# Optimization experiments

Measured on AMD Instinct MI355X. Metric: run time of the kernel, lower is better.

Reference implementation:

```python
import jax, jax.numpy as jnp
import numpy as np

N, C, H, T, D, K = 4096, 512, 128, 64, 20, 10


def setup_inputs() -> dict:
    key = jax.random.key(0)
    ks = jax.random.split(key, 40)
    s = 0.05
    inp = {}
    inp["x"] = jax.random.normal(ks[0], (N, D * T), jnp.float32)
    inp["concept_matrix"] = (jax.random.uniform(ks[1], (N, C)) < 0.05).astype(jnp.float32)
    inp["market_value"] = jax.random.uniform(ks[2], (N,), jnp.float32) + 0.1
    # GRU params (torch layout: w_ih [3H,in], w_hh [3H,H], biases [3H]); 2 layers
    inp["gru_w_ih0"] = jax.random.normal(ks[3], (3 * H, D), jnp.float32) * s
    inp["gru_w_hh0"] = jax.random.normal(ks[4], (3 * H, H), jnp.float32) * s
    inp["gru_b_ih0"] = jax.random.normal(ks[5], (3 * H,), jnp.float32) * s
    inp["gru_b_hh0"] = jax.random.normal(ks[6], (3 * H,), jnp.float32) * s
    inp["gru_w_ih1"] = jax.random.normal(ks[7], (3 * H, H), jnp.float32) * s
    inp["gru_w_hh1"] = jax.random.normal(ks[8], (3 * H, H), jnp.float32) * s
    inp["gru_b_ih1"] = jax.random.normal(ks[9], (3 * H,), jnp.float32) * s
    inp["gru_b_hh1"] = jax.random.normal(ks[10], (3 * H,), jnp.float32) * s
    names = ["ps", "hs", "ps_fore", "hs_fore", "ps_back", "hs_back", "indi"]
    for i, n in enumerate(names):
        inp["w_" + n] = jax.random.normal(ks[11 + 2 * i], (H, H), jnp.float32) * s
        inp["b_" + n] = jax.random.normal(ks[12 + 2 * i], (H,), jnp.float32) * s
    inp["w_out"] = jax.random.normal(ks[30], (1, H), jnp.float32) * s
    inp["b_out"] = jax.random.normal(ks[31], (1,), jnp.float32) * s
    return inp


def _cos_sim(x, y):
    # x [n,d], y [m,d] -> [n,m]; NaN (0/0) replaced by 0 via safe denominator
    xy = x @ y.T
    nx = jnp.sqrt(jnp.sum(x * x, axis=1))[:, None]
    ny = jnp.sqrt(jnp.sum(y * y, axis=1))[:, None]
    return xy / jnp.maximum(nx @ ny.T, 1e-12)


def _gru_layer(seq, wih, whh, bih, bhh):
    # seq [T, n, in] -> outputs [T, n, H]
    n = seq.shape[1]
    h0 = jnp.zeros((n, whh.shape[1]), seq.dtype)

    def step(h, xt):
        gx = xt @ wih.T + bih
        gh = h @ whh.T + bhh
        gxr, gxz, gxn = jnp.split(gx, 3, axis=1)
        ghr, ghz, ghn = jnp.split(gh, 3, axis=1)
        r = jax.nn.sigmoid(gxr + ghr)
        z = jax.nn.sigmoid(gxz + ghz)
        ncand = jnp.tanh(gxn + r * ghn)
        hnew = (1.0 - z) * ncand + z * h
        return hnew, hnew

    _, out = jax.lax.scan(step, h0, seq)
    return out


def reference(x, concept_matrix, market_value,
              gru_w_ih0, gru_w_hh0, gru_b_ih0, gru_b_hh0,
              gru_w_ih1, gru_w_hh1, gru_b_ih1, gru_b_hh1,
              w_ps, b_ps, w_hs, b_hs, w_ps_fore, b_ps_fore, w_hs_fore, b_hs_fore,
              w_ps_back, b_ps_back, w_hs_back, b_hs_back, w_indi, b_indi,
              w_out, b_out):
    n = x.shape[0]
    # [n, D*T] -> [n, D, T] -> [n, T, D] -> [T, n, D]
    seq = jnp.swapaxes(x.reshape(n, D, -1).transpose(0, 2, 1), 0, 1)
    out0 = _gru_layer(seq, gru_w_ih0, gru_w_hh0, gru_b_ih0, gru_b_hh0)
    out1 = _gru_layer(out0, gru_w_ih1, gru_w_hh1, gru_b_ih1, gru_b_hh1)
    x_hidden = out1[-1]  # [n, H]

    # --- predefined-concept branch ---
    s2c = concept_matrix * market_value[:, None]
    s2c_den = jnp.sum(s2c, axis=0)[None, :] * concept_matrix + 1.0
    s2c = s2c / s2c_den
    hidden = s2c.T @ x_hidden  # [C, H]
    v1 = jnp.sum(hidden, axis=1) != 0  # valid concepts (replaces row filtering)
    s2c2 = jax.nn.softmax(x_hidden @ hidden.T, axis=0)  # [n, C], column-wise
    hidden2 = s2c2.T @ x_hidden  # [C, H]
    c2s = _cos_sim(x_hidden, hidden2)
    c2s = jax.nn.softmax(jnp.where(v1[None, :], c2s, -1e9), axis=1) * v1[None, :]
    p_shared = c2s @ hidden2
    p_shared = p_shared @ w_ps.T + b_ps
    p_back = p_shared @ w_ps_back.T + b_ps_back
    out_ps = jax.nn.leaky_relu(p_shared @ w_ps_fore.T + b_ps_fore)

    # --- hidden-concept branch ---
    h_shared = x_hidden - p_back
    hs2c = _cos_sim(h_shared, h_shared)  # [n, n]
    diag = jnp.diagonal(hs2c)
    hs2c = hs2c * (1.0 - jnp.eye(n, dtype=hs2c.dtype))
    _, idx = jax.lax.top_k(hs2c, K)  # [n, K]
    mask = jnp.zeros_like(hs2c).at[jnp.arange(n)[:, None], idx].set(1.0)
    hs2c = hs2c * mask
    hs2c = hs2c + jnp.diag((jnp.sum(hs2c, axis=0) != 0).astype(hs2c.dtype) * diag)
    hidden_h = (h_shared.T @ hs2c).T  # [n, H]
    v2 = jnp.sum(hidden_h, axis=1) != 0
    hc2s = _cos_sim(h_shared, hidden_h)
    hc2s = jax.nn.softmax(jnp.where(v2[None, :], hc2s, -1e9), axis=1) * v2[None, :]
    h_si = hc2s @ hidden_h
    h_si = h_si @ w_hs.T + b_hs
    h_back = h_si @ w_hs_back.T + b_hs_back
    out_hs = jax.nn.leaky_relu(h_si @ w_hs_fore.T + b_hs_fore)

    # --- individual branch + head ---
    indi = x_hidden - p_back - h_back
    out_indi = jax.nn.leaky_relu(indi @ w_indi.T + b_indi)
    all_info = out_ps + out_hs + out_indi
    return (all_info @ w_out.T + b_out).squeeze()
```

## Files before the change

### kernel.cpp

```cpp
#include <hip/hip_runtime.h>
#include <cstddef>

#define NR 4096
#define CDIM 512
#define HDIM 128
#define TSTEPS 64
#define DDIM 20
#define KTOP 10

typedef __attribute__((ext_vector_type(8))) short short8;
typedef __attribute__((ext_vector_type(4))) float f32x4;

__device__ __forceinline__ unsigned short f2bf(float f) {
    union { float f; unsigned u; } x; x.f = f;
    unsigned r = (x.u + 0x7fffu + ((x.u >> 16) & 1u)) >> 16;
    return (unsigned short)r;
}
__device__ __forceinline__ unsigned short f2bf_t(float f) {
    union { float f; unsigned u; } x; x.f = f;
    return (unsigned short)(x.u >> 16);
}
__device__ __forceinline__ float bf2f(unsigned short h) {
    union { unsigned u; float f; } x; x.u = ((unsigned)h) << 16;
    return x.f;
}
__device__ __forceinline__ float sigm(float v) {
    return __builtin_amdgcn_rcpf(1.f + __expf(-v));
}
__device__ __forceinline__ float tanh_f(float v) {
    return 1.f - 2.f * __builtin_amdgcn_rcpf(1.f + __expf(2.f * v));
}

#define MFMA16(a, b, c) __builtin_amdgcn_mfma_f32_16x16x32_bf16(a, b, c, 0, 0, 0)

struct MG {
    const float* A; const unsigned short* Bh; const unsigned short* Bl;
    const float* bias; float* C; const float* aux; float* sub;
    const unsigned short* Ah; const unsigned short* Al;
    int N, K, kchunk, flags;
};

__global__ __launch_bounds__(256) void mfma_gemm(MG g)
{
    const int tid = threadIdx.x;
    const int w = tid >> 6, lane = tid & 63, quad = lane >> 4, lm = lane & 15;
    const int bm = (blockIdx.y << 6) + (w << 4);
    const int bn = blockIdx.x << 6;
    const int NC = g.K >> 5;
    const int c0 = (blockIdx.z * g.kchunk) >> 5;
    const int c1 = c0 + (g.kchunk >> 5);
    const float* arow = g.A + (size_t)(bm + lm) * g.K;
    const int packA = g.flags & 16;
    f32x4 acc[4];
    #pragma unroll
    for (int t = 0; t < 4; t++) acc[t] = (f32x4){0.f, 0.f, 0.f, 0.f};

    for (int c = c0; c < c1; c++) {
        short8 ah, al;
        if (packA) {
            size_t aidx = ((size_t)((bm >> 4) * NC + c) * 64 + lane) * 8;
            ah = *(const short8*)(g.Ah + aidx);
            al = *(const short8*)(g.Al + aidx);
        } else {
            const float* ap = arow + (c << 5) + (quad << 3);
            float4 a0 = *(const float4*)ap;
            float4 a1 = *(const float4*)(ap + 4);
            #pragma unroll
            for (int jj = 0; jj < 4; jj++) {
                float f = (&a0.x)[jj];
                unsigned short h = f2bf(f);
                ah[jj] = h; al[jj] = f2bf_t(f - bf2f(h));
                f = (&a1.x)[jj];
                h = f2bf(f);
                ah[4 + jj] = h; al[4 + jj] = f2bf_t(f - bf2f(h));
            }
        }
        #pragma unroll
        for (int t = 0; t < 4; t++) {
            size_t bidx = ((size_t)(((bn >> 4) + t) * NC + c) * 64 + lane) * 8;
            short8 bh = *(const short8*)(g.Bh + bidx);
            short8 bl = *(const short8*)(g.Bl + bidx);
            acc[t] = MFMA16(ah, bh, acc[t]);
            acc[t] = MFMA16(ah, bl, acc[t]);
            acc[t] = MFMA16(al, bh, acc[t]);
        }
    }
    #pragma unroll
    for (int t = 0; t < 4; t++) {
        #pragma unroll
        for (int rg = 0; rg < 4; rg++) {
            int row = bm + (quad << 2) + rg;
            int col = bn + (t << 4) + lm;
            float v = acc[t][rg];
            if (g.flags & 1) v += g.bias[col];
            if (g.flags & 2) v = v > 0.f ? v : 0.01f * v;
            if (g.flags & 4) atomicAdd(&g.C[(size_t)row * g.N + col], v);
            else g.C[(size_t)row * g.N + col] = v;
            if (g.flags & 8)
                g.sub[(size_t)row * g.N + col] = g.aux[(size_t)row * g.N + col] - v;
        }
    }
}

__global__ void pack_bt(const float* __restrict__ src, unsigned short* __restrict__ hi,
                        unsigned short* __restrict__ lo, int K, int total)
{
    int idx = blockIdx.x * 256 + threadIdx.x;
    if (idx >= total) return;
    int NC = K >> 5;
    int lane = idx & 63;
    int c = (idx >> 6) % NC;
    int t = idx / (NC * 64);
    int n = (t << 4) + (lane & 15);
    int kb = (c << 5) + ((lane >> 4) << 3);
    #pragma unroll
    for (int j = 0; j < 8; j++) {
        float f = src[(size_t)n * K + kb + j];
        unsigned short h = f2bf(f);
        hi[(size_t)idx * 8 + j] = h;
        lo[(size_t)idx * 8 + j] = f2bf_t(f - bf2f(h));
    }
}

__global__ void pack_both(const float* __restrict__ src,
                          unsigned short* __restrict__ bth, unsigned short* __restrict__ btl,
                          unsigned short* __restrict__ knh, unsigned short* __restrict__ knl,
                          int N, int total_kn)
{
    int idx = blockIdx.x * 256 + threadIdx.x;
    int lane = idx & 63;
    int totBT = (N >> 4) * 256;
    if (idx < totBT) {
        int c = (idx >> 6) & 3;
        int t = idx >> 8;
        int n = (t << 4) + (lane & 15);
        int kb = (c << 5) + ((lane >> 4) << 3);
        #pragma unroll
        for (int j = 0; j < 8; j++) {
            float f = src[(size_t)n * HDIM + kb + j];
            unsigned short h = f2bf(f);
            bth[(size_t)idx * 8 + j] = h;
            btl[(size_t)idx * 8 + j] = f2bf_t(f - bf2f(h));
        }
    }
    if (idx < total_kn) {
        int NC = N >> 5;
        int c = (idx >> 6) % NC;
        int t = idx / (NC * 64);
        int n = (t << 4) + (lane & 15);
        int kb = (c << 5) + ((lane >> 4) << 3);
        #pragma unroll
        for (int j = 0; j < 8; j++) {
            float f = src[(size_t)(kb + j) * HDIM + n];
            unsigned short h = f2bf(f);
            knh[(size_t)idx * 8 + j] = h;
            knl[(size_t)idx * 8 + j] = f2bf_t(f - bf2f(h));
        }
    }
}

struct W7 {
    const float* src[7];
    unsigned short* hi[7];
    unsigned short* lo[7];
};
__global__ void pack_w7(W7 p)
{
    int idx = blockIdx.x * 256 + threadIdx.x;
    if (idx >= 7 * 2048) return;
    int m = idx >> 11;
    int r = idx & 2047;
    int lane = r & 63;
    int c = (r >> 6) & 3;
    int t = r >> 8;
    int n = (t << 4) + (lane & 15);
    int kb = (c << 5) + ((lane >> 4) << 3);
    const float* src = p.src[m];
    unsigned short* hi = p.hi[m];
    unsigned short* lo = p.lo[m];
    #pragma unroll
    for (int j = 0; j < 8; j++) {
        float f = src[(size_t)n * HDIM + kb + j];
        unsigned short h = f2bf(f);
        hi[(size_t)r * 8 + j] = h;
        lo[(size_t)r * 8 + j] = f2bf_t(f - bf2f(h));
    }
}

__global__ __launch_bounds__(256) void scan_topk(const float* __restrict__ S,
        const float* __restrict__ hn, float* __restrict__ diagv,
        float* __restrict__ tvals, int* __restrict__ tidx)
{
    int row = blockIdx.x;
    const float* d = S + (size_t)row * NR;
    int tid = threadIdx.x;
    int wv = tid >> 6, lane = tid & 63;
    float hi_ = hn[row];
    float lv[16];
    #pragma unroll
    for (int i = 0; i < 16; i++) {
        int j = tid + (i << 8);
        float v = d[j] / fmaxf(hi_ * hn[j], 1e-12f);
        if (j == row) { diagv[row] = v; v = 0.f; }
        lv[i] = v;
    }
    __shared__ float sv[4];
    __shared__ int si[4];
    for (int k = 0; k < KTOP; k++) {
        float bv = -INFINITY; int bi = 0x7fffffff;
        #pragma unroll
        for (int i = 0; i < 16; i++) {
            int j = tid + (i << 8);
            if (lv[i] > bv || (lv[i] == bv && j < bi)) { bv = lv[i]; bi = j; }
        }
        #pragma unroll
        for (int m = 1; m < 64; m <<= 1) {
            float ov = __shfl_xor(bv, m); int oi = __shfl_xor(bi, m);
            if (ov > bv || (ov == bv && oi < bi)) { bv = ov; bi = oi; }
        }
        if (lane == 0) { sv[wv] = bv; si[wv] = bi; }
        __syncthreads();
        bv = sv[0]; bi = si[0];
        #pragma unroll
        for (int w = 1; w < 4; w++) {
            float ov = sv[w]; int oi = si[w];
            if (ov > bv || (ov == bv && oi < bi)) { bv = ov; bi = oi; }
        }
        if (tid == 0) { tvals[row * KTOP + k] = bv; tidx[row * KTOP + k] = bi; }
        if ((bi & 255) == tid) lv[bi >> 8] = -INFINITY;
        __syncthreads();
    }
}

__global__ __launch_bounds__(512) void hc2s_flash(
    const float* __restrict__ hsh, const float* __restrict__ hn,
    const float* __restrict__ hhn, const float* __restrict__ v2,
    const unsigned short* __restrict__ Bh, const unsigned short* __restrict__ Bl,
    const unsigned short* __restrict__ Vh, const unsigned short* __restrict__ Vl,
    float* __restrict__ pO, float* __restrict__ pM, float* __restrict__ pL)
{
    __shared__ __attribute__((aligned(16))) unsigned short Ph[8][16 * 72];
    __shared__ __attribute__((aligned(16))) unsigned short Plo[8][16 * 72];

    const int tid = threadIdx.x;
    const int wv = tid >> 6, lane = tid & 63, quad = lane >> 4, lm = lane & 15;
    const int rg2 = wv >> 1;
    const int cc = wv & 1;
    const int bm = (blockIdx.x << 6) + (rg2 << 4);
    const int rgg = (blockIdx.x << 2) + rg2;
    const int pidx = (blockIdx.y << 1) + cc;
    const int jt0 = (blockIdx.y << 4) + (cc << 3);

    short8 ahh[4], ahl[4];
    #pragma unroll
    for (int c = 0; c < 4; c++) {
        const float* ap = hsh + (size_t)(bm + lm) * HDIM + (c << 5) + (quad << 3);
        float4 a0 = *(const float4*)ap;
        float4 a1 = *(const float4*)(ap + 4);
        #pragma unroll
        for (int j = 0; j < 4; j++) {
            float f = (&a0.x)[j];
            unsigned short h = f2bf(f);
            ahh[c][j] = h; ahl[c][j] = f2bf_t(f - bf2f(h));
            f = (&a1.x)[j];
            h = f2bf(f);
            ahh[c][4 + j] = h; ahl[c][4 + j] = f2bf_t(f - bf2f(h));
        }
    }
    float hnr[4];
    #pragma unroll
    for (int rg = 0; rg < 4; rg++) hnr[rg] = hn[bm + (quad << 2) + rg];

    float m_old[4], l_old[4];
    #pragma unroll
    for (int rg = 0; rg < 4; rg++) { m_old[rg] = -INFINITY; l_old[rg] = 0.f; }
    f32x4 o[8];
    #pragma unroll
    for (int vt = 0; vt < 8; vt++) o[vt] = (f32x4){0.f, 0.f, 0.f, 0.f};

    const int pwr = lm * 72;
    for (int it = 0; it < 8; it++) {
        const int jt = jt0 + it;
        f32x4 s[4];
        #pragma unroll
        for (int tg = 0; tg < 4; tg++) {
            s[tg] = (f32x4){0.f, 0.f, 0.f, 0.f};
            #pragma unroll
            for (int c = 0; c < 4; c++) {
                size_t bidx = ((size_t)(((jt << 2) + tg) * 4 + c) * 64 + lane) * 8;
                short8 bh = *(const short8*)(Bh + bidx);
                short8 bl = *(const short8*)(Bl + bidx);
                s[tg] = MFMA16(ahh[c], bh, s[tg]);
                s[tg] = MFMA16(ahh[c], bl, s[tg]);
                s[tg] = MFMA16(ahl[c], bh, s[tg]);
            }
        }
        float sv[4][4];
        #pragma unroll
        for (int tg = 0; tg < 4; tg++) {
            int col = (jt << 6) + (tg << 4) + lm;
            float hc = hhn[col];
            float vm = v2[col];
            #pragma unroll
            for (int rg = 0; rg < 4; rg++) {
                float v = s[tg][rg] * __builtin_amdgcn_rcpf(fmaxf(hnr[rg] * hc, 1e-12f));
                sv[tg][rg] = (vm == 0.f) ? -1e9f : v;
            }
        }
        float m_new[4], alpha[4], tsum[4], pv[4][4];
        #pragma unroll
        for (int rg = 0; rg < 4; rg++) {
            float m = fmaxf(fmaxf(sv[0][rg], sv[1][rg]), fmaxf(sv[2][rg], sv[3][rg]));
            #pragma unroll
            for (int d = 1; d < 16; d <<= 1) m = fmaxf(m, __shfl_xor(m, d));
            m_new[rg] = fmaxf(m_old[rg], m);
            alpha[rg] = __expf(m_old[rg] - m_new[rg]);
        }
        #pragma unroll
        for (int rg = 0; rg < 4; rg++) {
            float p0_ = __expf(sv[0][rg] - m_new[rg]);
            float p1_ = __expf(sv[1][rg] - m_new[rg]);
            float p2_ = __expf(sv[2][rg] - m_new[rg]);
            float p3_ = __expf(sv[3][rg] - m_new[rg]);
            pv[0][rg] = p0_; pv[1][rg] = p1_; pv[2][rg] = p2_; pv[3][rg] = p3_;
            float ss = p0_ + p1_ + p2_ + p3_;
            #pragma unroll
            for (int d = 1; d < 16; d <<= 1) ss += __shfl_xor(ss, d);
            tsum[rg] = ss;
        }
        #pragma unroll
        for (int rg = 0; rg < 4; rg++) {
            l_old[rg] = l_old[rg] * alpha[rg] + tsum[rg];
            m_old[rg] = m_new[rg];
        }
        #pragma unroll
        for (int vt = 0; vt < 8; vt++) {
            #pragma unroll
            for (int rg = 0; rg < 4; rg++) o[vt][rg] *= alpha[rg];
        }
        #pragma unroll
        for (int tg = 0; tg < 4; tg++) {
            #pragma unroll
            for (int rg = 0; rg < 4; rg++) {
                int off = ((quad << 2) + rg) * 72 + (tg << 4) + lm;
                float p = pv[tg][rg];
                unsigned short h = f2bf(p);
                Ph[wv][off] = h;
                Plo[wv][off] = f2bf_t(p - bf2f(h));
            }
        }
        __asm__ volatile("s_waitcnt lgkmcnt(0)" ::: "memory");
        #pragma unroll
        for (int c2 = 0; c2 < 2; c2++) {
            int poff = pwr + (c2 << 5) + (quad << 3);
            short8 pah = *(const short8*)&Ph[wv][poff];
            short8 pal = *(const short8*)&Plo[wv][poff];
            int cg = (jt << 1) + c2;
            #pragma unroll
            for (int vt = 0; vt < 8; vt++) {
                size_t b0 = ((size_t)(vt * 128 + cg) * 64 + lane) * 8;
                short8 vh = *(const short8*)(Vh + b0);
                short8 vl = *(const short8*)(Vl + b0);
                o[vt] = MFMA16(pah, vh, o[vt]);
                o[vt] = MFMA16(pah, vl, o[vt]);
                o[vt] = MFMA16(pal, vh, o[vt]);
            }
        }
    }
    size_t pb = ((size_t)rgg * 8 + pidx) * 16;
    #pragma unroll
    for (int rg = 0; rg < 4; rg++) {
        int r = (quad << 2) + rg;
        #pragma unroll
        for (int vt = 0; vt < 8; vt++)
            pO[(pb + r) * 128 + (vt << 4) + lm] = o[vt][rg];
    }
    if (lm == 0) {
        #pragma unroll
        for (int rg = 0; rg < 4; rg++) {
            int r = (quad << 2) + rg;
            pM[pb + r] = m_old[rg];
            pL[pb + r] = l_old[rg];
        }
    }
}

__global__ __launch_bounds__(256) void hc2s_merge(const float* __restrict__ pO,
        const float* __restrict__ pM, const float* __restrict__ pL,
        float* __restrict__ O)
{
    int rgg = blockIdx.x;
    int tid = threadIdx.x;
    int r = tid >> 4;
    int c0 = (tid & 15) << 3;
    float m[8], e[8];
    float M = -INFINITY;
    #pragma unroll
    for (int i = 0; i < 8; i++) {
        m[i] = pM[((size_t)rgg * 8 + i) * 16 + r];
        M = fmaxf(M, m[i]);
    }
    float L = 0.f;
    #pragma unroll
    for (int i = 0; i < 8; i++) {
        e[i] = __expf(m[i] - M);
        L += pL[((size_t)rgg * 8 + i) * 16 + r] * e[i];
    }
    float invL = __builtin_amdgcn_rcpf(L);
    float a[8];
    #pragma unroll
    for (int k = 0; k < 8; k++) a[k] = 0.f;
    #pragma unroll
    for (int i = 0; i < 8; i++) {
        const float* src = pO + (((size_t)rgg * 8 + i) * 16 + r) * 128 + c0;
        float4 v0 = *(const float4*)src;
        float4 v1 = *(const float4*)(src + 4);
        a[0] += v0.x * e[i]; a[1] += v0.y * e[i]; a[2] += v0.z * e[i]; a[3] += v0.w * e[i];
        a[4] += v1.x * e[i]; a[5] += v1.y * e[i]; a[6] += v1.z * e[i]; a[7] += v1.w * e[i];
    }
    float* dst = O + ((size_t)rgg * 16 + r) * 128 + c0;
    #pragma unroll
    for (int k = 0; k < 8; k++) dst[k] = a[k] * invL;
}

__global__ void pack_wb(const float* __restrict__ W, unsigned short* __restrict__ Wp,
                        int K, int nch)
{
    int idx = blockIdx.x * 256 + threadIdx.x;
    if (idx >= 24 * nch * 64) return;
    int lane = idx & 63;
    int c = (idx >> 6) % nch;
    int t = idx / (nch * 64);
    int n = t * 16 + (lane & 15);
    int kb = c * 32 + (lane >> 4) * 8;
    #pragma unroll
    for (int j = 0; j < 8; j++) {
        int k = kb + j;
        float f = (k < K) ? W[(size_t)n * K + k] : 0.f;
        Wp[(size_t)idx * 8 + j] = f2bf(f);
    }
}

__global__ void seq_transpose(const float* __restrict__ x, unsigned* __restrict__ seq)
{
    int idx = blockIdx.x * 256 + threadIdx.x;
    int d = idx % DDIM;
    int r = idx / DDIM;
    int n = r & (NR - 1);
    int t = r >> 12;
    float v = x[(size_t)n * (DDIM * TSTEPS) + d * TSTEPS + t];
    unsigned short h = f2bf(v);
    unsigned short l = f2bf_t(v - bf2f(h));
    seq[idx] = (unsigned)h | ((unsigned)l << 16);
}

__global__ __launch_bounds__(512) void gru_mfma(
    const unsigned* __restrict__ seq,
    const unsigned short* __restrict__ wih0p,
    const unsigned short* __restrict__ whh0p,
    const unsigned short* __restrict__ wih1p,
    const unsigned short* __restrict__ whh1p,
    const float* __restrict__ bih0, const float* __restrict__ bhh0,
    const float* __restrict__ bih1, const float* __restrict__ bhh1,
    float* __restrict__ xh)
{
    __shared__ __attribute__((aligned(16))) unsigned short hA[2][2][2][16 * 136];
    __shared__ __attribute__((aligned(16))) unsigned short xA[2][2][16 * 40];

    const int tid = threadIdx.x;
    const int w2 = tid >> 6;
    const int lane = tid & 63;
    const int quad = lane >> 4;
    const int lm = lane & 15;
    const int n0 = blockIdx.x << 4;
    const int j = (w2 << 4) + lm;

    for (int i = tid; i < 2 * 2 * 2 * 16 * 136; i += 512) ((unsigned short*)hA)[i] = 0;
    for (int i = tid; i < 2 * 2 * 16 * 40; i += 512) ((unsigned short*)xA)[i] = 0;

    float br0 = bih0[j] + bhh0[j];
    float bz0 = bih0[128 + j] + bhh0[128 + j];
    float bni0 = bih0[256 + j];
    float bnh0 = bhh0[256 + j];
    float br1 = bih1[j] + bhh1[j];
    float bz1 = bih1[128 + j] + bhh1[128 + j];
    float bni1 = bih1[256 + j];
    float bnh1 = bhh1[256 + j];

    short8 W0x[3], W0h[3][4], W1x[3][4], W1h[3][4];
    {
        const int lb = lane * 8;
        W0x[0] = *(const short8*)&wih0p[(size_t)(w2) * 512 + lb];
        W0x[1] = *(const short8*)&wih0p[(size_t)(8 + w2) * 512 + lb];
        W0x[2] = *(const short8*)&wih0p[(size_t)(16 + w2) * 512 + lb];
        #pragma unroll
        for (int c = 0; c < 4; c++) {
            W0h[0][c] = *(const short8*)&whh0p[(size_t)((w2) * 4 + c) * 512 + lb];
            W0h[1][c] = *(const short8*)&whh0p[(size_t)((8 + w2) * 4 + c) * 512 + lb];
            W0h[2][c] = *(const short8*)&whh0p[(size_t)((16 + w2) * 4 + c) * 512 + lb];
            W1x[0][c] = *(const short8*)&wih1p[(size_t)((w2) * 4 + c) * 512 + lb];
            W1x[1][c] = *(const short8*)&wih1p[(size_t)((8 + w2) * 4 + c) * 512 + lb];
            W1x[2][c] = *(const short8*)&wih1p[(size_t)((16 + w2) * 4 + c) * 512 + lb];
            W1h[0][c] = *(const short8*)&whh1p[(size_t)((w2) * 4 + c) * 512 + lb];
            W1h[1][c] = *(const short8*)&whh1p[(size_t)((8 + w2) * 4 + c) * 512 + lb];
            W1h[2][c] = *(const short8*)&whh1p[(size_t)((16 + w2) * 4 + c) * 512 + lb];
        }
    }

    const int aoff = lm * 136 + quad * 8;
    const int xoff = lm * 40 + quad * 8;
    const bool stager = tid < 16 * DDIM;
    const int soff = stager ? (tid / DDIM) * 40 + (tid % DDIM) : 0;

    const unsigned* sp = seq + (size_t)n0 * DDIM;
    if (stager) {
        unsigned v = sp[tid];
        xA[0][0][soff] = (unsigned short)(v & 0xffffu);
        xA[0][1][soff] = (unsigned short)(v >> 16);
    }
    sp += (size_t)NR * DDIM;
    __syncthreads();

#define GRU_STEP(B, RB, LAST)                                                     \
{                                                                                 \
    unsigned xv = 0;                                                              \
    if (!(LAST) && stager) xv = sp[tid];             \
    f32x4 accr = (f32x4){0.f, 0.f, 0.f, 0.f};                                     \
    f32x4 accz = (f32x4){0.f, 0.f, 0.f, 0.f};                                     \
    f32x4 accni = (f32x4){0.f, 0.f, 0.f, 0.f};                                    \
    f32x4 accnh = (f32x4){0.f, 0.f, 0.f, 0.f};                                    \
                              \
    {                                                                             \
        short8 axh = *(const short8*)&xA[B][0][xoff];                             \
        short8 axl = *(const short8*)&xA[B][1][xoff];                             \
        accr = MFMA16(axh, W0x[0], accr);                                         \
        accr = MFMA16(axl, W0x[0], accr);                                         \
        accz = MFMA16(axh, W0x[1], accz);                                         \
        accz = MFMA16(axl, W0x[1], accz);                                         \
        accni = MFMA16(axh, W0x[2], accni);                                       \
        accni = MFMA16(axl, W0x[2], accni);                                       \
    }                                                                             \
    _Pragma("unroll")                                                             \
    for (int c = 0; c < 4; c++) {                                                 \
        short8 ahh = *(const short8*)&hA[RB][0][0][aoff + c * 32];                \
        short8 ahl = *(const short8*)&hA[RB][0][1][aoff + c * 32];                \
        accr = MFMA16(ahh, W0h[0][c], accr);                                      \
        accr = MFMA16(ahl, W0h[0][c], accr);                                      \
        accz = MFMA16(ahh, W0h[1][c], accz);                                      \
        accz = MFMA16(ahl, W0h[1][c], accz);                                      \
        accnh = MFMA16(ahh, W0h[2][c], accnh);                                    \
        accnh = MFMA16(ahl, W0h[2][c], accnh);                                    \
    }                                                                             \
    float hold[4];                                                                \
    _Pragma("unroll")                                                             \
    for (int rg = 0; rg < 4; rg++) {                                              \
        int off = (quad * 4 + rg) * 136 + j;                                      \
        hold[rg] = bf2f(hA[RB][0][0][off]) + bf2f(hA[RB][0][1][off]);             \
    }                                                                             \
         \
    _Pragma("unroll")                                                             \
    for (int rg = 0; rg < 4; rg++) {                                              \
        float r = sigm(accr[rg] + br0);                                           \
        float z = sigm(accz[rg] + bz0);                                           \
        float nc = tanh_f(accni[rg] + bni0 + r * (accnh[rg] + bnh0));             \
        float hnew = nc + z * (hold[rg] - nc);                                    \
        int off = (quad * 4 + rg) * 136 + j;                                      \
        unsigned short hh_ = f2bf(hnew);                                          \
        hA[B][0][0][off] = hh_;                                                   \
        hA[B][0][1][off] = f2bf_t(hnew - bf2f(hh_));                              \
    }                                                                             \
    if (!(LAST) && stager) {                                                      \
        xA[RB][0][soff] = (unsigned short)(xv & 0xffffu);                         \
        xA[RB][1][soff] = (unsigned short)(xv >> 16);                             \
    }                                                                             \
    __syncthreads();                \
                   \
    accr = (f32x4){0.f, 0.f, 0.f, 0.f};                                           \
    accz = (f32x4){0.f, 0.f, 0.f, 0.f};                                           \
    accni = (f32x4){0.f, 0.f, 0.f, 0.f};                                          \
    accnh = (f32x4){0.f, 0.f, 0.f, 0.f};                                          \
    _Pragma("unroll")                                                             \
    for (int c = 0; c < 4; c++) {                                                 \
        short8 a0h = *(const short8*)&hA[B][0][0][aoff + c * 32];                 \
        short8 a0l = *(const short8*)&hA[B][0][1][aoff + c * 32];                 \
        short8 a1h = *(const short8*)&hA[RB][1][0][aoff + c * 32];                \
        short8 a1l = *(const short8*)&hA[RB][1][1][aoff + c * 32];                \
        accr = MFMA16(a0h, W1x[0][c], accr);                                      \
        accr = MFMA16(a0l, W1x[0][c], accr);                                      \
        accr = MFMA16(a1h, W1h[0][c], accr);                                      \
        accr = MFMA16(a1l, W1h[0][c], accr);                                      \
        accz = MFMA16(a0h, W1x[1][c], accz);                                      \
        accz = MFMA16(a0l, W1x[1][c], accz);                                      \
        accz = MFMA16(a1h, W1h[1][c], accz);                                      \
        accz = MFMA16(a1l, W1h[1][c], accz);                                      \
        accni = MFMA16(a0h, W1x[2][c], accni);                                    \
        accni = MFMA16(a0l, W1x[2][c], accni);                                    \
        accnh = MFMA16(a1h, W1h[2][c], accnh);                                    \
        accnh = MFMA16(a1l, W1h[2][c], accnh);                                    \
    }                                                                             \
    _Pragma("unroll")                                                             \
    for (int rg = 0; rg < 4; rg++) {                                              \
        int off = (quad * 4 + rg) * 136 + j;                                      \
        hold[rg] = bf2f(hA[RB][1][0][off]) + bf2f(hA[RB][1][1][off]);             \
    }                                                                             \
         \
    _Pragma("unroll")                                                             \
    for (int rg = 0; rg < 4; rg++) {                                              \
        float r = sigm(accr[rg] + br1);                                           \
        float z = sigm(accz[rg] + bz1);                                           \
        float nc = tanh_f(accni[rg] + bni1 + r * (accnh[rg] + bnh1));             \
        float hnew = nc + z * (hold[rg] - nc);                                    \
        int off = (quad * 4 + rg) * 136 + j;                                      \
        unsigned short hh_ = f2bf(hnew);                                          \
        hA[B][1][0][off] = hh_;                                                   \
        hA[B][1][1][off] = f2bf_t(hnew - bf2f(hh_));                              \
        if (LAST)                                                                 \
            xh[(size_t)(n0 + quad * 4 + rg) * HDIM + j] = hnew;                   \
    }                                                                             \
    sp += (size_t)NR * DDIM;                                                      \
}

    for (int t = 0; t < TSTEPS - 2; t += 2) {
        GRU_STEP(0, 1, false)
        GRU_STEP(1, 0, false)
    }
    GRU_STEP(0, 1, false)
    GRU_STEP(1, 0, true)
#undef GRU_STEP
}

__global__ __launch_bounds__(256) void den_atomic(const float* __restrict__ cm,
        const float* __restrict__ mv, float* __restrict__ den)
{
    int c = blockIdx.x * 64 + (threadIdx.x & 63);
    int rg = threadIdx.x >> 6;
    int nbase = blockIdx.y * 128;
    float acc = 0.f;
    for (int i = 0; i < 32; i++) {
        int n = nbase + rg + (i << 2);
        acc += cm[(size_t)n * CDIM + c] * mv[n];
    }
    __shared__ float red[4][64];
    red[rg][threadIdx.x & 63] = acc;
    __syncthreads();
    if (rg == 0)
        atomicAdd(&den[c], red[0][threadIdx.x] + red[1][threadIdx.x] +
                           red[2][threadIdx.x] + red[3][threadIdx.x]);
}

__global__ __launch_bounds__(256) void s2ct_trans(const float* __restrict__ cm,
        const float* __restrict__ mv, const float* __restrict__ den,
        float* __restrict__ s2cT)
{
    __shared__ float tile[64][65];
    __shared__ float mvs[64];
    const int tid = threadIdx.x;
    const int n0 = blockIdx.x << 6;
    const int c0 = blockIdx.y << 6;
    const int lc = tid & 63, lr = tid >> 6;
    if (tid < 64) mvs[tid] = mv[n0 + tid];
    #pragma unroll
    for (int i = 0; i < 16; i++) {
        int n = lr + (i << 2);
        tile[n][lc] = cm[(size_t)(n0 + n) * CDIM + c0 + lc];
    }
    __syncthreads();
    #pragma unroll
    for (int i = 0; i < 16; i++) {
        int c = lr + (i << 2);
        float m = tile[lc][c];
        float d = den[c0 + c];
        s2cT[(size_t)(c0 + c) * NR + n0 + lc] = (m * mvs[lc]) / (d * m + 1.f);
    }
}

__global__ void row_norm(const float* __restrict__ a, float* __restrict__ out)
{
    int r = blockIdx.x;
    float acc = 0.f;
    for (int h = threadIdx.x; h < HDIM; h += 64) {
        float v = a[(size_t)r * HDIM + h];
        acc += v * v;
    }
    for (int o = 32; o > 0; o >>= 1) acc += __shfl_down(acc, o);
    if (threadIdx.x == 0) out[r] = sqrtf(acc);
}

__global__ void row_nonzero(const float* __restrict__ a, float* __restrict__ out)
{
    int r = blockIdx.x;
    float acc = 0.f;
    for (int h = threadIdx.x; h < HDIM; h += 64) acc += a[(size_t)r * HDIM + h];
    for (int o = 32; o > 0; o >>= 1) acc += __shfl_down(acc, o);
    if (threadIdx.x == 0) out[r] = (acc != 0.f) ? 1.f : 0.f;
}

__global__ void row_norm_nz(const float* __restrict__ a, float* __restrict__ nrm,
                            float* __restrict__ nz)
{
    int r = blockIdx.x;
    float acc = 0.f, s = 0.f;
    for (int h = threadIdx.x; h < HDIM; h += 64) {
        float v = a[(size_t)r * HDIM + h];
        acc += v * v;
        s += v;
    }
    for (int o = 32; o > 0; o >>= 1) { acc += __shfl_down(acc, o); s += __shfl_down(s, o); }
    if (threadIdx.x == 0) { nrm[r] = sqrtf(acc); nz[r] = (s != 0.f) ? 1.f : 0.f; }
}

__global__ __launch_bounds__(256) void cos_softmax_row(float* __restrict__ data, int N,
        const float* __restrict__ rn, const float* __restrict__ cn,
        const float* __restrict__ vmask)
{
    int row = blockIdx.x;
    float* d = data + (size_t)row * N;
    int tid = threadIdx.x;
    int wv = tid >> 6, lane = tid & 63;
    __shared__ float red[8];
    float rnv = rn ? rn[row] : 0.f;
    float mx = -INFINITY;
    for (int j = tid; j < N; j += 256) {
        float v = d[j];
        if (cn) v = v * __builtin_amdgcn_rcpf(fmaxf(rnv * cn[j], 1e-12f));
        if (vmask && vmask[j] == 0.f) v = -1e9f;
        d[j] = v;
        mx = fmaxf(mx, v);
    }
    #pragma unroll
    for (int m = 1; m < 64; m <<= 1) mx = fmaxf(mx, __shfl_xor(mx, m));
    if (lane == 0) red[wv] = mx;
    __syncthreads();
    float M = fmaxf(fmaxf(red[0], red[1]), fmaxf(red[2], red[3]));
    float sum = 0.f;
    for (int j = tid; j < N; j += 256) {
        float e = __expf(d[j] - M);
        d[j] = e;
        sum += e;
    }
    #pragma unroll
    for (int m = 1; m < 64; m <<= 1) sum += __shfl_xor(sum, m);
    if (lane == 0) red[4 + wv] = sum;
    __syncthreads();
    float inv = __builtin_amdgcn_rcpf(red[4] + red[5] + red[6] + red[7]);
    for (int j = tid; j < N; j += 256) {
        float v = d[j] * inv;
        if (vmask) v *= vmask[j];
        d[j] = v;
    }
}

__global__ void colsum_scatter(const float* __restrict__ vals, const int* __restrict__ idxs,
                               float* __restrict__ colsum)
{
    int idx = blockIdx.x * 256 + threadIdx.x;
    if (idx < NR * KTOP) atomicAdd(&colsum[idxs[idx]], vals[idx]);
}

__global__ void hh_scatter(const float* __restrict__ vals, const int* __restrict__ idxs,
                           const float* __restrict__ hsh, float* __restrict__ hh)
{
    int p = blockIdx.x;
    int j = idxs[p];
    float v = vals[p];
    int i = p / KTOP;
    atomicAdd(&hh[(size_t)j * HDIM + threadIdx.x], v * hsh[(size_t)i * HDIM + threadIdx.x]);
}

__global__ void hh_diag(const float* __restrict__ colsum, const float* __restrict__ diag,
                        const float* __restrict__ hsh, float* __restrict__ hh)
{
    int idx = blockIdx.x * 256 + threadIdx.x;
    int j = idx >> 7;
    if (colsum[j] != 0.f) hh[idx] += diag[j] * hsh[idx];
}

__global__ void head_kernel(const float* __restrict__ ps, const float* __restrict__ hs,
                            const float* __restrict__ indi, const float* __restrict__ w,
                            const float* __restrict__ b, float* __restrict__ out)
{
    int n = blockIdx.x;
    int t = threadIdx.x;
    float acc = 0.f;
    for (int h = t; h < HDIM; h += 64) {
        size_t k = (size_t)n * HDIM + h;
        acc += (ps[k] + hs[k] + indi[k]) * w[h];
    }
    for (int o = 32; o > 0; o >>= 1) acc += __shfl_down(acc, o);
    if (t == 0) out[n] = acc + b[0];
}

static inline void mg(hipStream_t s, const float* A, const unsigned short* Bh,
                      const unsigned short* Bl, const float* bias, float* C,
                      int M, int N, int K, int z, int flags,
                      const float* aux = nullptr, float* sub = nullptr,
                      const unsigned short* Ah = nullptr, const unsigned short* Al = nullptr)
{
    MG g{A, Bh, Bl, bias, C, aux, sub, Ah, Al, N, K, K / z,
         flags | (z > 1 ? 4 : 0) | (Ah ? 16 : 0)};
    mfma_gemm<<<dim3(N / 64, M / 64, z), 256, 0, s>>>(g);
}
static inline void pbt(hipStream_t s, const float* src, unsigned short* hi,
                       unsigned short* lo, int N, int K)
{
    int total = (N / 16) * (K / 32) * 64;
    pack_bt<<<(total + 255) / 256, 256, 0, s>>>(src, hi, lo, K, total);
}
static inline void pboth(hipStream_t s, const float* src,
                         unsigned short* bth, unsigned short* btl,
                         unsigned short* knh, unsigned short* knl, int N)
{
    int totBT = (N / 16) * 4 * 64;
    int totKN = 8 * (N / 32) * 64;
    int tot = totBT > totKN ? totBT : totKN;
    pack_both<<<(tot + 255) / 256, 256, 0, s>>>(src, bth, btl, knh, knl, N, totKN);
}

extern "C" void kernel_launch(void* const* d_in, const int* in_sizes, int n_in,
                              void* d_out, int out_size, void* d_ws, size_t ws_size,
                              hipStream_t stream)
{
    (void)in_sizes; (void)n_in; (void)out_size; (void)ws_size;
    const float* x    = (const float*)d_in[0];
    const float* cm   = (const float*)d_in[1];
    const float* mv   = (const float*)d_in[2];
    const float* wih0 = (const float*)d_in[3];
    const float* whh0 = (const float*)d_in[4];
    const float* bih0 = (const float*)d_in[5];
    const float* bhh0 = (const float*)d_in[6];
    const float* wih1 = (const float*)d_in[7];
    const float* whh1 = (const float*)d_in[8];
    const float* bih1 = (const float*)d_in[9];
    const float* bhh1 = (const float*)d_in[10];
    const float* w_ps = (const float*)d_in[11];
    const float* b_ps = (const float*)d_in[12];
    const float* w_hs = (const float*)d_in[13];
    const float* b_hs = (const float*)d_in[14];
    const float* w_ps_fore = (const float*)d_in[15];
    const float* b_ps_fore = (const float*)d_in[16];
    const float* w_hs_fore = (const float*)d_in[17];
    const float* b_hs_fore = (const float*)d_in[18];
    const float* w_ps_back = (const float*)d_in[19];
    const float* b_ps_back = (const float*)d_in[20];
    const float* w_hs_back = (const float*)d_in[21];
    const float* b_hs_back = (const float*)d_in[22];
    const float* w_indi = (const float*)d_in[23];
    const float* b_indi = (const float*)d_in[24];
    const float* w_out  = (const float*)d_in[25];
    const float* b_out  = (const float*)d_in[26];
    float* out = (float*)d_out;

    float* ws = (float*)d_ws;
    float* BIG = ws;
    float* h0 = ws + 16777216;
    float* h1 = h0 + 524288;
    float* den = h1 + 524288;
    float* v1 = den + 512;
    float* hidden = v1 + 512;
    float* hidden2 = hidden + 65536;
    float* xnorm = hidden2 + 65536;
    float* h2n = xnorm + 4096;
    float* p0 = h2n + 512;
    float* p_shared = p0 + 524288;
    float* p_back = p_shared + 524288;
    float* out_ps = p_back + 524288;
    float* h_shared = out_ps + 524288;
    float* hn = h_shared + 524288;
    float* diagv = hn + 4096;
    float* colsum = diagv + 4096;
    float* tvals = colsum + 4096;
    int*   tidx = (int*)(tvals + 40960);
    float* hidden_h = (float*)(tidx + 40960);
    float* v2 = hidden_h + 524288;
    float* hhn = v2 + 4096;
    float* hsi0 = hhn + 4096;
    float* h_si = hsi0 + 524288;
    float* h_back = h_si + 524288;
    float* out_hs = h_back + 524288;
    float* indi = out_hs + 524288;
    float* out_indi = indi + 524288;
    float* extra = out_indi + 524288;

    unsigned* seqt = (unsigned*)BIG;
    unsigned short* wih0p = (unsigned short*)(BIG + 5242880);
    unsigned short* whh0p = wih0p + 12288;
    unsigned short* wih1p = whh0p + 49152;
    unsigned short* whh1p = wih1p + 49152;
    float* s2cT = BIG;
    float* L    = BIG + 2097152;
    float* c2s  = BIG + 4194304;
    unsigned short* PB = (unsigned short*)(BIG + 6291456);
    unsigned short* pbt_xh_hi = PB;
    unsigned short* pbt_xh_lo = pbt_xh_hi + 524288;
    unsigned short* pkn_xh_hi = pbt_xh_lo + 524288;
    unsigned short* pkn_xh_lo = pkn_xh_hi + 524288;
    unsigned short* pbt_h2_hi = pkn_xh_lo + 524288;
    unsigned short* pbt_h2_lo = pbt_h2_hi + 65536;
    unsigned short* pkn_h2_hi = pbt_h2_lo + 65536;
    unsigned short* pkn_h2_lo = pkn_h2_hi + 65536;
    unsigned short* wps_hi  = pkn_h2_lo + 65536;
    unsigned short* wps_lo  = wps_hi + 16384;
    unsigned short* wpsb_hi = wps_lo + 16384;
    unsigned short* wpsb_lo = wpsb_hi + 16384;
    unsigned short* wpsf_hi = wpsb_lo + 16384;
    unsigned short* wpsf_lo = wpsf_hi + 16384;
    unsigned short* pbt_hsh_hi = (unsigned short*)p0;
    unsigned short* pbt_hsh_lo = pbt_hsh_hi + 524288;
    unsigned short* pbt_hh_hi = (unsigned short*)indi;
    unsigned short* pbt_hh_lo = pbt_hh_hi + 524288;
    unsigned short* pkn_hh_hi = (unsigned short*)out_indi;
    unsigned short* pkn_hh_lo = pkn_hh_hi + 524288;
    float* part_O = BIG;
    float* part_m = BIG + 4194304;
    float* part_l = BIG + 4227072;
    unsigned short* EX = (unsigned short*)extra;
    unsigned short* whs_hi  = EX;            unsigned short* whs_lo  = EX + 16384;
    unsigned short* whsb_hi = EX + 32768;    unsigned short* whsb_lo = EX + 49152;
    unsigned short* whsf_hi = EX + 65536;    unsigned short* whsf_lo = EX + 81920;
    unsigned short* wind_hi = EX + 98304;    unsigned short* wind_lo = EX + 114688;

    seq_transpose<<<(TSTEPS * NR * DDIM) / 256, 256, 0, stream>>>(x, seqt);
    pack_wb<<<6, 256, 0, stream>>>(wih0, wih0p, DDIM, 1);
    pack_wb<<<24, 256, 0, stream>>>(whh0, whh0p, HDIM, 4);
    pack_wb<<<24, 256, 0, stream>>>(wih1, wih1p, HDIM, 4);
    pack_wb<<<24, 256, 0, stream>>>(whh1, whh1p, HDIM, 4);
    {
        W7 w7;
        w7.src[0] = w_ps;      w7.hi[0] = wps_hi;  w7.lo[0] = wps_lo;
        w7.src[1] = w_ps_back; w7.hi[1] = wpsb_hi; w7.lo[1] = wpsb_lo;
        w7.src[2] = w_ps_fore; w7.hi[2] = wpsf_hi; w7.lo[2] = wpsf_lo;
        w7.src[3] = w_hs;      w7.hi[3] = whs_hi;  w7.lo[3] = whs_lo;
        w7.src[4] = w_hs_back; w7.hi[4] = whsb_hi; w7.lo[4] = whsb_lo;
        w7.src[5] = w_hs_fore; w7.hi[5] = whsf_hi; w7.lo[5] = whsf_lo;
        w7.src[6] = w_indi;    w7.hi[6] = wind_hi; w7.lo[6] = wind_lo;
        pack_w7<<<56, 256, 0, stream>>>(w7);
    }
    gru_mfma<<<NR / 16, 512, 0, stream>>>(seqt, wih0p, whh0p, wih1p, whh1p,
                                          bih0, bhh0, bih1, bhh1, h1);
    float* x_hidden = h1;

    hipMemsetAsync(den, 0, CDIM * sizeof(float), stream);
    den_atomic<<<dim3(CDIM / 64, 32), 256, 0, stream>>>(cm, mv, den);
    s2ct_trans<<<dim3(NR / 64, CDIM / 64), 256, 0, stream>>>(cm, mv, den, s2cT);
    pboth(stream, x_hidden, pbt_xh_hi, pbt_xh_lo, pkn_xh_hi, pkn_xh_lo, NR);
    hipMemsetAsync(hidden, 0, 65536 * sizeof(float), stream);
    mg(stream, s2cT, pkn_xh_hi, pkn_xh_lo, nullptr, hidden, CDIM, HDIM, NR, 8, 0);
    row_nonzero<<<CDIM, 64, 0, stream>>>(hidden, v1);
    mg(stream, hidden, pbt_xh_hi, pbt_xh_lo, nullptr, L, CDIM, NR, HDIM, 1, 0);
    cos_softmax_row<<<CDIM, 256, 0, stream>>>(L, NR, nullptr, nullptr, nullptr);
    hipMemsetAsync(hidden2, 0, 65536 * sizeof(float), stream);
    mg(stream, L, pkn_xh_hi, pkn_xh_lo, nullptr, hidden2, CDIM, HDIM, NR, 8, 0);
    row_norm<<<NR, 64, 0, stream>>>(x_hidden, xnorm);
    row_norm<<<CDIM, 64, 0, stream>>>(hidden2, h2n);
    pboth(stream, hidden2, pbt_h2_hi, pbt_h2_lo, pkn_h2_hi, pkn_h2_lo, CDIM);
    mg(stream, x_hidden, pbt_h2_hi, pbt_h2_lo, nullptr, c2s, NR, CDIM, HDIM, 1, 0,
       nullptr, nullptr, pbt_xh_hi, pbt_xh_lo);
    cos_softmax_row<<<NR, 256, 0, stream>>>(c2s, CDIM, xnorm, h2n, v1);
    hipMemsetAsync(p0, 0, 524288 * sizeof(float), stream);
    mg(stream, c2s, pkn_h2_hi, pkn_h2_lo, nullptr, p0, NR, HDIM, CDIM, 2, 0);
    mg(stream, p0, wps_hi, wps_lo, b_ps, p_shared, NR, HDIM, HDIM, 1, 1);
    mg(stream, p_shared, wpsb_hi, wpsb_lo, b_ps_back, p_back, NR, HDIM, HDIM, 1, 1 | 8,
       x_hidden, h_shared);
    mg(stream, p_shared, wpsf_hi, wpsf_lo, b_ps_fore, out_ps, NR, HDIM, HDIM, 1, 1 | 2);

    row_norm<<<NR, 64, 0, stream>>>(h_shared, hn);
    pbt(stream, h_shared, pbt_hsh_hi, pbt_hsh_lo, NR, HDIM);
    mg(stream, h_shared, pbt_hsh_hi, pbt_hsh_lo, nullptr, BIG, NR, NR, HDIM, 1, 0,
       nullptr, nullptr, pbt_hsh_hi, pbt_hsh_lo);
    scan_topk<<<NR, 256, 0, stream>>>(BIG, hn, diagv, tvals, tidx);
    hipMemsetAsync(colsum, 0, NR * sizeof(float), stream);
    hipMemsetAsync(hidden_h, 0, 524288 * sizeof(float), stream);
    colsum_scatter<<<(NR * KTOP + 255) / 256, 256, 0, stream>>>(tvals, tidx, colsum);
    hh_scatter<<<NR * KTOP, HDIM, 0, stream>>>(tvals, tidx, h_shared, hidden_h);
    hh_diag<<<2048, 256, 0, stream>>>(colsum, diagv, h_shared, hidden_h);
    row_norm_nz<<<NR, 64, 0, stream>>>(hidden_h, hhn, v2);
    pboth(stream, hidden_h, pbt_hh_hi, pbt_hh_lo, pkn_hh_hi, pkn_hh_lo, NR);
    hc2s_flash<<<dim3(NR / 64, 4), 512, 0, stream>>>(h_shared, hn, hhn, v2,
                                                     pbt_hh_hi, pbt_hh_lo,
                                                     pkn_hh_hi, pkn_hh_lo,
                                                     part_O, part_m, part_l);
    hc2s_merge<<<NR / 16, 256, 0, stream>>>(part_O, part_m, part_l, hsi0);
    mg(stream, hsi0, whs_hi, whs_lo, b_hs, h_si, NR, HDIM, HDIM, 1, 1);
    mg(stream, h_si, whsb_hi, whsb_lo, b_hs_back, h_back, NR, HDIM, HDIM, 1, 1 | 8,
       h_shared, indi);
    mg(stream, h_si, whsf_hi, whsf_lo, b_hs_fore, out_hs, NR, HDIM, HDIM, 1, 1 | 2);

    mg(stream, indi, wind_hi, wind_lo, b_indi, out_indi, NR, HDIM, HDIM, 1, 1 | 2);
    head_kernel<<<NR, 64, 0, stream>>>(out_ps, out_hs, out_indi, w_out, b_out, out);
}
```

Baseline: 771.8 us.

## Skew GRU layers into one barrier per step and read x directly

Reorganises the 2-layer GRU recurrence so layer 0 at step t+1 and layer 1 at step t are computed in the same iteration, halving the __syncthreads count per timestep. It keeps the previous hidden states in registers instead of re-reading them from LDS, folds biases into accumulator initialisation, and drops the separate seq_transpose kernel by having stager threads load and split x directly with strided global reads. Rounding of the hi part changes from round-to-nearest to truncation, and launch_bounds now requests 2 blocks per CU, which may limit registers for the many weight fragments held per thread.

```diff
diff --git a/kernel.cpp b/kernel.cpp
--- a/kernel.cpp
+++ b/kernel.cpp
@@ -441,21 +441,8 @@
     }
 }
 
-__global__ void seq_transpose(const float* __restrict__ x, unsigned* __restrict__ seq)
-{
-    int idx = blockIdx.x * 256 + threadIdx.x;
-    int d = idx % DDIM;
-    int r = idx / DDIM;
-    int n = r & (NR - 1);
-    int t = r >> 12;
-    float v = x[(size_t)n * (DDIM * TSTEPS) + d * TSTEPS + t];
-    unsigned short h = f2bf(v);
-    unsigned short l = f2bf_t(v - bf2f(h));
-    seq[idx] = (unsigned)h | ((unsigned)l << 16);
-}
-
-__global__ __launch_bounds__(512) void gru_mfma(
-    const unsigned* __restrict__ seq,
+__global__ __launch_bounds__(512, 2) void gru_mfma(
+    const float* __restrict__ xg,
     const unsigned short* __restrict__ wih0p,
     const unsigned short* __restrict__ whh0p,
     const unsigned short* __restrict__ wih1p,
@@ -464,7 +451,8 @@
     const float* __restrict__ bih1, const float* __restrict__ bhh1,
     float* __restrict__ xh)
 {
-    __shared__ __attribute__((aligned(16))) unsigned short hA[2][2][2][16 * 136];
+    __shared__ __attribute__((aligned(16))) unsigned short h0A[2][2][16 * 136];
+    __shared__ __attribute__((aligned(16))) unsigned short h1A[2][2][16 * 136];
     __shared__ __attribute__((aligned(16))) unsigned short xA[2][2][16 * 40];
 
     const int tid = threadIdx.x;
@@ -475,7 +463,10 @@
     const int n0 = blockIdx.x << 4;
     const int j = (w2 << 4) + lm;
 
-    for (int i = tid; i < 2 * 2 * 2 * 16 * 136; i += 512) ((unsigned short*)hA)[i] = 0;
+    for (int i = tid; i < 2 * 2 * 16 * 136; i += 512) {
+        ((unsigned short*)h0A)[i] = 0;
+        ((unsigned short*)h1A)[i] = 0;
+    }
     for (int i = tid; i < 2 * 2 * 16 * 40; i += 512) ((unsigned short*)xA)[i] = 0;
 
     float br0 = bih0[j] + bhh0[j];
@@ -510,123 +501,143 @@
     const int aoff = lm * 136 + quad * 8;
     const int xoff = lm * 40 + quad * 8;
     const bool stager = tid < 16 * DDIM;
-    const int soff = stager ? (tid / DDIM) * 40 + (tid % DDIM) : 0;
-
-    const unsigned* sp = seq + (size_t)n0 * DDIM;
+    const int sn = tid / DDIM, sd = tid % DDIM;
+    const float* xrow = xg + (size_t)(n0 + sn) * (DDIM * TSTEPS) + sd * TSTEPS;
+    const int soff = sn * 40 + sd;
+
+    float h0reg[4] = {0.f, 0.f, 0.f, 0.f};
+    float h1reg[4] = {0.f, 0.f, 0.f, 0.f};
+
     if (stager) {
-        unsigned v = sp[tid];
-        xA[0][0][soff] = (unsigned short)(v & 0xffffu);
-        xA[0][1][soff] = (unsigned short)(v >> 16);
-    }
-    sp += (size_t)NR * DDIM;
+        float v0 = xrow[0], v1 = xrow[1];
+        unsigned short a = f2bf_t(v0);
+        xA[0][0][soff] = a; xA[0][1][soff] = f2bf_t(v0 - bf2f(a));
+        unsigned short b = f2bf_t(v1);
+        xA[1][0][soff] = b; xA[1][1][soff] = f2bf_t(v1 - bf2f(b));
+    }
     __syncthreads();
 
-#define GRU_STEP(B, RB, LAST)                                                     \
+    {
+        f32x4 accr = (f32x4){br0, br0, br0, br0};
+        f32x4 accz = (f32x4){bz0, bz0, bz0, bz0};
+        f32x4 accni = (f32x4){bni0, bni0, bni0, bni0};
+        short8 axh = *(const short8*)&xA[0][0][xoff];
+        short8 axl = *(const short8*)&xA[0][1][xoff];
+        accr = MFMA16(axh, W0x[0], accr);
+        accr = MFMA16(axl, W0x[0], accr);
+        accz = MFMA16(axh, W0x[1], accz);
+        accz = MFMA16(axl, W0x[1], accz);
+        accni = MFMA16(axh, W0x[2], accni);
+        accni = MFMA16(axl, W0x[2], accni);
+        #pragma unroll
+        for (int rg = 0; rg < 4; rg++) {
+            float r = sigm(accr[rg]);
+            float z = sigm(accz[rg]);
+            float nc = tanh_f(accni[rg] + r * bnh0);
+            float hnew = nc - z * nc;
+            h0reg[rg] = hnew;
+            int off = (quad * 4 + rg) * 136 + j;
+            unsigned short hh_ = f2bf_t(hnew);
+            h0A[0][0][off] = hh_;
+            h0A[0][1][off] = f2bf_t(hnew - bf2f(hh_));
+        }
+    }
+    __syncthreads();
+
+#define GRU_IT(B, DO_L0, XT, LAST)                                                \
 {                                                                                 \
-    unsigned xv = 0;                                                              \
-    if (!(LAST) && stager) xv = sp[tid];             \
-    f32x4 accr = (f32x4){0.f, 0.f, 0.f, 0.f};                                     \
-    f32x4 accz = (f32x4){0.f, 0.f, 0.f, 0.f};                                     \
-    f32x4 accni = (f32x4){0.f, 0.f, 0.f, 0.f};                                    \
-    f32x4 accnh = (f32x4){0.f, 0.f, 0.f, 0.f};                                    \
-                              \
-    {                                                                             \
-        short8 axh = *(const short8*)&xA[B][0][xoff];                             \
-        short8 axl = *(const short8*)&xA[B][1][xoff];                             \
-        accr = MFMA16(axh, W0x[0], accr);                                         \
-        accr = MFMA16(axl, W0x[0], accr);                                         \
-        accz = MFMA16(axh, W0x[1], accz);                                         \
-        accz = MFMA16(axl, W0x[1], accz);                                         \
-        accni = MFMA16(axh, W0x[2], accni);                                       \
-        accni = MFMA16(axl, W0x[2], accni);                                       \
+    float xv = 0.f;                                                               \
+    if ((XT) >= 0 && stager) xv = xrow[XT];          \
+    f32x4 accr0 = (f32x4){br0, br0, br0, br0};                                    \
+    f32x4 accz0 = (f32x4){bz0, bz0, bz0, bz0};                                    \
+    f32x4 accni0 = (f32x4){bni0, bni0, bni0, bni0};                               \
+    f32x4 accnh0 = (f32x4){bnh0, bnh0, bnh0, bnh0};                               \
+    f32x4 accr1 = (f32x4){br1, br1, br1, br1};                                    \
+    f32x4 accz1 = (f32x4){bz1, bz1, bz1, bz1};                                    \
+    f32x4 accni1 = (f32x4){bni1, bni1, bni1, bni1};                               \
+    f32x4 accnh1 = (f32x4){bnh1, bnh1, bnh1, bnh1};                               \
+    if (DO_L0) {                                                                  \
+        short8 axh = *(const short8*)&xA[(B) ^ 1][0][xoff];                       \
+        short8 axl = *(const short8*)&xA[(B) ^ 1][1][xoff];                       \
+        accr0 = MFMA16(axh, W0x[0], accr0);                                       \
+        accr0 = MFMA16(axl, W0x[0], accr0);                                       \
+        accz0 = MFMA16(axh, W0x[1], accz0);                                       \
+        accz0 = MFMA16(axl, W0x[1], accz0);                                       \
+        accni0 = MFMA16(axh, W0x[2], accni0);                                     \
+        accni0 = MFMA16(axl, W0x[2], accni0);                                     \
     }                                                                             \
     _Pragma("unroll")                                                             \
     for (int c = 0; c < 4; c++) {                                                 \
-        short8 ahh = *(const short8*)&hA[RB][0][0][aoff + c * 32];                \
-        short8 ahl = *(const short8*)&hA[RB][0][1][aoff + c * 32];                \
-        accr = MFMA16(ahh, W0h[0][c], accr);                                      \
-        accr = MFMA16(ahl, W0h[0][c], accr);                                      \
-        accz = MFMA16(ahh, W0h[1][c], accz);                                      \
-        accz = MFMA16(ahl, W0h[1][c], accz);                                      \
-        accnh = MFMA16(ahh, W0h[2][c], accnh);                                    \
-        accnh = MFMA16(ahl, W0h[2][c], accnh);                                    \
+        short8 a0h = *(const short8*)&h0A[B][0][aoff + c * 32];                   \
+        short8 a0l = *(const short8*)&h0A[B][1][aoff + c * 32];                   \
+        if (DO_L0) {                                                              \
+            accr0 = MFMA16(a0h, W0h[0][c], accr0);                                \
+            accr0 = MFMA16(a0l, W0h[0][c], accr0);                                \
+            accz0 = MFMA16(a0h, W0h[1][c], accz0);                                \
+            accz0 = MFMA16(a0l, W0h[1][c], accz0);                                \
+            accnh0 = MFMA16(a0h, W0h[2][c], accnh0);                              \
+            accnh0 = MFMA16(a0l, W0h[2][c], accnh0);                              \
+        }                                                                         \
+        accr1 = MFMA16(a0h, W1x[0][c], accr1);                                    \
+        accr1 = MFMA16(a0l, W1x[0][c], accr1);                                    \
+        accz1 = MFMA16(a0h, W1x[1][c], accz1);                                    \
+        accz1 = MFMA16(a0l, W1x[1][c], accz1);                                    \
+        accni1 = MFMA16(a0h, W1x[2][c], accni1);                                  \
+        accni1 = MFMA16(a0l, W1x[2][c], accni1);                                  \
+        short8 a1h = *(const short8*)&h1A[(B) ^ 1][0][aoff + c * 32];             \
+        short8 a1l = *(const short8*)&h1A[(B) ^ 1][1][aoff + c * 32];             \
+        accr1 = MFMA16(a1h, W1h[0][c], accr1);                                    \
+        accr1 = MFMA16(a1l, W1h[0][c], accr1);                                    \
+        accz1 = MFMA16(a1h, W1h[1][c], accz1);                                    \
+        accz1 = MFMA16(a1l, W1h[1][c], accz1);                                    \
+        accnh1 = MFMA16(a1h, W1h[2][c], accnh1);                                  \
+        accnh1 = MFMA16(a1l, W1h[2][c], accnh1);                                  \
     }                                                                             \
-    float hold[4];                                                                \
-    _Pragma("unroll")                                                             \
-    for (int rg = 0; rg < 4; rg++) {                                              \
-        int off = (quad * 4 + rg) * 136 + j;                                      \
-        hold[rg] = bf2f(hA[RB][0][0][off]) + bf2f(hA[RB][0][1][off]);             \
-    }                                                                             \
-         \
-    _Pragma("unroll")                                                             \
-    for (int rg = 0; rg < 4; rg++) {                                              \
-        float r = sigm(accr[rg] + br0);                                           \
-        float z = sigm(accz[rg] + bz0);                                           \
-        float nc = tanh_f(accni[rg] + bni0 + r * (accnh[rg] + bnh0));             \
-        float hnew = nc + z * (hold[rg] - nc);                                    \
-        int off = (quad * 4 + rg) * 136 + j;                                      \
-        unsigned short hh_ = f2bf(hnew);                                          \
-        hA[B][0][0][off] = hh_;                                                   \
-        hA[B][0][1][off] = f2bf_t(hnew - bf2f(hh_));                              \
-    }                                                                             \
-    if (!(LAST) && stager) {                                                      \
-        xA[RB][0][soff] = (unsigned short)(xv & 0xffffu);                         \
-        xA[RB][1][soff] = (unsigned short)(xv >> 16);                             \
-    }                                                                             \
-    __syncthreads();                \
-                   \
-    accr = (f32x4){0.f, 0.f, 0.f, 0.f};                                           \
-    accz = (f32x4){0.f, 0.f, 0.f, 0.f};                                           \
-    accni = (f32x4){0.f, 0.f, 0.f, 0.f};                                          \
-    accnh = (f32x4){0.f, 0.f, 0.f, 0.f};                                          \
-    _Pragma("unroll")                                                             \
-    for (int c = 0; c < 4; c++) {                                                 \
-        short8 a0h = *(const short8*)&hA[B][0][0][aoff + c * 32];                 \
-        short8 a0l = *(const short8*)&hA[B][0][1][aoff + c * 32];                 \
-        short8 a1h = *(const short8*)&hA[RB][1][0][aoff + c * 32];                \
-        short8 a1l = *(const short8*)&hA[RB][1][1][aoff + c * 32];                \
-        accr = MFMA16(a0h, W1x[0][c], accr);                                      \
-        accr = MFMA16(a0l, W1x[0][c], accr);                                      \
-        accr = MFMA16(a1h, W1h[0][c], accr);                                      \
-        accr = MFMA16(a1l, W1h[0][c], accr);                                      \
-        accz = MFMA16(a0h, W1x[1][c], accz);                                      \
-        accz = MFMA16(a0l, W1x[1][c], accz);                                      \
-        accz = MFMA16(a1h, W1h[1][c], accz);                                      \
-        accz = MFMA16(a1l, W1h[1][c], accz);                                      \
-        accni = MFMA16(a0h, W1x[2][c], accni);                                    \
-        accni = MFMA16(a0l, W1x[2][c], accni);                                    \
-        accnh = MFMA16(a1h, W1h[2][c], accnh);                                    \
-        accnh = MFMA16(a1l, W1h[2][c], accnh);                                    \
+    if (DO_L0) {                                                                  \
+        _Pragma("unroll")                                                         \
+        for (int rg = 0; rg < 4; rg++) {                                          \
+            float r = sigm(accr0[rg]);                                            \
+            float z = sigm(accz0[rg]);                                            \
+            float nc = tanh_f(accni0[rg] + r * accnh0[rg]);                       \
+            float hnew = nc + z * (h0reg[rg] - nc);                               \
+            h0reg[rg] = hnew;                                                     \
+            int off = (quad * 4 + rg) * 136 + j;                                  \
+            unsigned short hh_ = f2bf_t(hnew);                                    \
+            h0A[(B) ^ 1][0][off] = hh_;                                           \
+            h0A[(B) ^ 1][1][off] = f2bf_t(hnew - bf2f(hh_));                      \
+        }                                                                         \
     }                                                                             \
     _Pragma("unroll")                                                             \
     for (int rg = 0; rg < 4; rg++) {                                              \
-        int off = (quad * 4 + rg) * 136 + j;                                      \
-        hold[rg] = bf2f(hA[RB][1][0][off]) + bf2f(hA[RB][1][1][off]);             \
+        float r = sigm(accr1[rg]);                                                \
+        float z = sigm(accz1[rg]);                                                \
+        float nc = tanh_f(accni1[rg] + r * accnh1[rg]);                           \
+        float hnew = nc + z * (h1reg[rg] - nc);                                   \
+        h1reg[rg] = hnew;                                                         \
+        if (LAST) {                                                               \
+            xh[(size_t)(n0 + quad * 4 + rg) * HDIM + j] = hnew;                   \
+        } else {                                                                  \
+            int off = (quad * 4 + rg) * 136 + j;                                  \
+            unsigned short hh_ = f2bf_t(hnew);                                    \
+            h1A[B][0][off] = hh_;                                                 \
+            h1A[B][1][off] = f2bf_t(hnew - bf2f(hh_));                            \
+        }                                                                         \
     }                                                                             \
-         \
-    _Pragma("unroll")                                                             \
-    for (int rg = 0; rg < 4; rg++) {                                              \
-        float r = sigm(accr[rg] + br1);                                           \
-        float z = sigm(accz[rg] + bz1);                                           \
-        float nc = tanh_f(accni[rg] + bni1 + r * (accnh[rg] + bnh1));             \
-        float hnew = nc + z * (hold[rg] - nc);                                    \
-        int off = (quad * 4 + rg) * 136 + j;                                      \
-        unsigned short hh_ = f2bf(hnew);                                          \
-        hA[B][1][0][off] = hh_;                                                   \
-        hA[B][1][1][off] = f2bf_t(hnew - bf2f(hh_));                              \
-        if (LAST)                                                                 \
-            xh[(size_t)(n0 + quad * 4 + rg) * HDIM + j] = hnew;                   \
+    if ((XT) >= 0 && stager) {                                                    \
+        unsigned short hh_ = f2bf_t(xv);                                          \
+        xA[B][0][soff] = hh_;                                                     \
+        xA[B][1][soff] = f2bf_t(xv - bf2f(hh_));                                  \
     }                                                                             \
-    sp += (size_t)NR * DDIM;                                                      \
-}
-
-    for (int t = 0; t < TSTEPS - 2; t += 2) {
-        GRU_STEP(0, 1, false)
-        GRU_STEP(1, 0, false)
-    }
-    GRU_STEP(0, 1, false)
-    GRU_STEP(1, 0, true)
-#undef GRU_STEP
+    if (!(LAST)) __syncthreads();                                                 \
+}
+
+    for (int i = 0; i < 62; i += 2) {
+        GRU_IT(0, true, i + 2, false)
+        GRU_IT(1, true, i + 3, false)
+    }
+    GRU_IT(0, true, -1, false)
+    GRU_IT(1, false, -1, true)
+#undef GRU_IT
 }
 
 __global__ __launch_bounds__(256) void den_atomic(const float* __restrict__ cm,
@@ -881,7 +892,6 @@
     float* out_indi = indi + 524288;
     float* extra = out_indi + 524288;
 
-    unsigned* seqt = (unsigned*)BIG;
     unsigned short* wih0p = (unsigned short*)(BIG + 5242880);
     unsigned short* whh0p = wih0p + 12288;
     unsigned short* wih1p = whh0p + 49152;
@@ -919,7 +929,6 @@
     unsigned short* whsf_hi = EX + 65536;    unsigned short* whsf_lo = EX + 81920;
     unsigned short* wind_hi = EX + 98304;    unsigned short* wind_lo = EX + 114688;
 
-    seq_transpose<<<(TSTEPS * NR * DDIM) / 256, 256, 0, stream>>>(x, seqt);
     pack_wb<<<6, 256, 0, stream>>>(wih0, wih0p, DDIM, 1);
     pack_wb<<<24, 256, 0, stream>>>(whh0, whh0p, HDIM, 4);
     pack_wb<<<24, 256, 0, stream>>>(wih1, wih1p, HDIM, 4);
@@ -935,7 +944,7 @@
         w7.src[6] = w_indi;    w7.hi[6] = wind_hi; w7.lo[6] = wind_lo;
         pack_w7<<<56, 256, 0, stream>>>(w7);
     }
-    gru_mfma<<<NR / 16, 512, 0, stream>>>(seqt, wih0p, whh0p, wih1p, whh1p,
+    gru_mfma<<<NR / 16, 512, 0, stream>>>(x, wih0p, whh0p, wih1p, whh1p,
                                           bih0, bhh0, bih1, bhh1, h1);
     float* x_hidden = h1;
 
```

Result: faster. 749.6 us (-2.9%).
